# Optimization experiments

Hardware: AMD Instinct MI355X
Metric: run time of the kernel (lower is better)

## Reference

```python
import jax, jax.numpy as jnp
import numpy as np

N_NODES = 100000
N_EDGES = 1600000
D_FEAT = 48


def setup_inputs() -> dict:
    key = jax.random.key(0)
    k1, k2, k3, k4 = jax.random.split(key, 4)
    rows = jax.random.randint(k1, (N_EDGES,), 0, N_NODES, dtype=jnp.int32)
    cols = jax.random.randint(k2, (N_EDGES,), 0, N_NODES, dtype=jnp.int32)
    # normalized adjacency values (positive, like D^-1/2 A D^-1/2 entries)
    vals = jax.random.uniform(k3, (N_EDGES,), dtype=jnp.float32)
    embeds = jax.random.normal(k4, (N_NODES, D_FEAT), dtype=jnp.float32)
    return {"rows": rows, "cols": cols, "vals": vals, "embeds": embeds}


def reference(rows, cols, vals, embeds):
    # torch.spmm(adj, embeds) with adj in COO form:
    # out[i] = sum_{e : rows[e]==i} vals[e] * embeds[cols[e]]
    msgs = vals[:, None] * embeds[cols]          # [E, D] gather + scale
    out = jax.ops.segment_sum(msgs, rows, num_segments=embeds.shape[0])  # [N, D]
    return out
```

## Files before the change

### kernel.cpp

```cpp
#include <hip/hip_runtime.h>


#define N_NODES 100000
#define D_FEAT 48
#define DQ (D_FEAT / 4)
#define DQ4 (D_FEAT / 8)

#define BUCKET_BITS 7
#define BUCKET_NODES 128
#define N_BUCKETS ((N_NODES + BUCKET_NODES - 1) / BUCKET_NODES)
#define CAPB 2432

#define CHUNK 8192
#define P1_THREADS 1024
#define VPT (CHUNK / P1_THREADS / 4)

#define P2_THREADS 768
#define EPT2 ((CAPB + P2_THREADS - 1) / P2_THREADS)
#define NG6 (P2_THREADS / 6)

#define OVF_CAP 4096
#define EBF_UINT2 (N_NODES * DQ)

typedef float  fl32x4 __attribute__((ext_vector_type(4)));
typedef unsigned long long u64;

__device__ __forceinline__ unsigned short f2bf(float f) {
    unsigned u = __float_as_uint(f);
    return (unsigned short)((u + 0x7FFFu + ((u >> 16) & 1u)) >> 16);
}

__device__ __forceinline__ float4 bf2f4(uint2 h) {
    float4 m;
    m.x = __uint_as_float((h.x & 0xFFFFu) << 16);
    m.y = __uint_as_float(h.x & 0xFFFF0000u);
    m.z = __uint_as_float((h.y & 0xFFFFu) << 16);
    m.w = __uint_as_float(h.y & 0xFFFF0000u);
    return m;
}

__global__ __launch_bounds__(P1_THREADS) void partition_kernel(
        const int* __restrict__ rows, const int* __restrict__ cols,
        const float* __restrict__ vals, int* __restrict__ gcur,
        uint2* __restrict__ tmp, uint4* __restrict__ ovf, int* __restrict__ novf,
        const float* __restrict__ embeds, uint2* __restrict__ ebf,
        int n_edges) {
    __shared__ int counts[N_BUCKETS];
    __shared__ int starts[N_BUCKETS];
    __shared__ int cursor[N_BUCKETS];
    __shared__ int adj[N_BUCKETS];
    __shared__ int wtot[16];
    __shared__ unsigned lkey[CHUNK];
    __shared__ unsigned lval[CHUNK];
    __shared__ int      ldst[CHUNK];

    int t = threadIdx.x;
    int lane = t & 63;
    int wid = t >> 6;
    int base = blockIdx.x * CHUNK;
    int n = min(CHUNK, n_edges - base);
    int n4 = n >> 2;

    for (int i = t; i < N_BUCKETS; i += P1_THREADS) counts[i] = 0;
    __syncthreads();

    int      b[VPT * 4];
    unsigned key[VPT * 4];
    float    v[VPT * 4];
    const int4*   rows4 = reinterpret_cast<const int4*>(rows + base);
    const int4*   cols4 = reinterpret_cast<const int4*>(cols + base);
    const float4* vals4 = reinterpret_cast<const float4*>(vals + base);
#pragma unroll
    for (int k = 0; k < VPT; ++k) {
        int idx4 = k * P1_THREADS + t;
        bool ok = idx4 < n4;
        int4   r4 = ok ? rows4[idx4] : make_int4(0, 0, 0, 0);
        int4   c4 = ok ? cols4[idx4] : make_int4(0, 0, 0, 0);
        float4 v4 = ok ? vals4[idx4] : make_float4(0.f, 0.f, 0.f, 0.f);
        int rr[4] = {r4.x, r4.y, r4.z, r4.w};
        int cc[4] = {c4.x, c4.y, c4.z, c4.w};
        float vv[4] = {v4.x, v4.y, v4.z, v4.w};
#pragma unroll
        for (int j = 0; j < 4; ++j) {
            int i = k * 4 + j;
            b[i] = -1;
            if (ok) {
                b[i] = rr[j] >> BUCKET_BITS;
                key[i] = ((unsigned)(rr[j] & (BUCKET_NODES - 1)) << 17) | (unsigned)cc[j];
                v[i] = vv[j];
                atomicAdd(&counts[b[i]], 1);
            }
        }
    }

    if (ebf) {
        const float4* e4 = reinterpret_cast<const float4*>(embeds);
        int stride = gridDim.x * P1_THREADS;
        for (int i = blockIdx.x * P1_THREADS + t; i < EBF_UINT2; i += stride) {
            float4 f = e4[i];
            uint2 p;
            p.x = (unsigned)f2bf(f.x) | ((unsigned)f2bf(f.y) << 16);
            p.y = (unsigned)f2bf(f.z) | ((unsigned)f2bf(f.w) << 16);
            ebf[i] = p;
        }
    }
    __syncthreads();

    int cnt_t = (t < N_BUCKETS) ? counts[t] : 0;
    int x = cnt_t;
#pragma unroll
    for (int d = 1; d < 64; d <<= 1) {
        int y = __shfl_up(x, d, 64);
        if (lane >= d) x += y;
    }
    if (lane == 63) wtot[wid] = x;
    __syncthreads();
    if (t < 64) {
        int w = (t < 16) ? wtot[t] : 0;
        int xs = w;
#pragma unroll
        for (int d = 1; d < 16; d <<= 1) {
            int y = __shfl_up(xs, d, 64);
            if (lane >= d) xs += y;
        }
        if (t < 16) wtot[t] = xs - w;
    }
    __syncthreads();
    if (t < N_BUCKETS) {
        int excl = x - cnt_t + wtot[wid];
        starts[t] = excl;
        cursor[t] = excl;
        int gp = (cnt_t > 0) ? atomicAdd(&gcur[t], cnt_t) : 0;
        adj[t] = t * CAPB + gp - excl;
    }
    __syncthreads();

#pragma unroll
    for (int i = 0; i < VPT * 4; ++i) {
        if (b[i] >= 0) {
            int p = atomicAdd(&cursor[b[i]], 1);
            int dest = adj[b[i]] + p;
            if (dest < (b[i] + 1) * CAPB) {
                lkey[p] = key[i];
                lval[p] = __float_as_uint(v[i]);
                ldst[p] = dest;
            } else {
                ldst[p] = -1;
                int o = atomicAdd(novf, 1);
                if (o < OVF_CAP) {
                    unsigned rl = key[i] >> 17;
                    ovf[o] = make_uint4((unsigned)b[i] * BUCKET_NODES + rl,
                                        key[i] & 0x1FFFFu, __float_as_uint(v[i]), 0u);
                }
            }
        }
    }
    __syncthreads();

    u64* tmp8 = reinterpret_cast<u64*>(tmp);
    for (int i = t; i < n; i += P1_THREADS) {
        int d = ldst[i];
        if (d >= 0)
            tmp8[d] = (u64)lkey[i] | ((u64)lval[i] << 32);
    }
}

#define ACCUM_OVF_TAIL(GATHER_EXPR)                                             \
    {                                                                           \
        int nov = min(*novf, OVF_CAP);                                          \
        if (nov > 0) {                                                          \
            __syncthreads();                                                    \
            int lo = bkt * BUCKET_NODES, hi = lo + BUCKET_NODES;                \
            for (int i = t; i < nov; i += P2_THREADS) {                         \
                uint4 en = ovf[i];                                              \
                int node = (int)en.x;                                           \
                if (node >= lo && node < hi && node < N_NODES) {                \
                    unsigned c = en.y;                                          \
                    float v = __uint_as_float(en.z);                            \
                    for (int qq = 0; qq < DQ; ++qq) {                           \
                        float4 m = GATHER_EXPR;                                 \
                        float* dst = out + (size_t)node * D_FEAT + qq * 4;      \
                        atomicAdd(dst + 0, v * m.x);                            \
                        atomicAdd(dst + 1, v * m.y);                            \
                        atomicAdd(dst + 2, v * m.z);                            \
                        atomicAdd(dst + 3, v * m.w);                            \
                    }                                                           \
                }                                                               \
            }                                                                   \
        }                                                                       \
    }

__global__ __launch_bounds__(P2_THREADS) void accum_bf16_kernel(
        const int* __restrict__ gcur, const uint2* __restrict__ tmp,
        const uint2* __restrict__ ebf, float* __restrict__ out,
        const int* __restrict__ novf, const uint4* __restrict__ ovf) {
    __shared__ uint2 sorted[CAPB];
    __shared__ int cnt[BUCKET_NODES];
    __shared__ int cur[BUCKET_NODES];
    __shared__ int roff[BUCKET_NODES + 1];
    __shared__ int ws2[2];

    int t = threadIdx.x;
    int lane = t & 63;
    int bkt = blockIdx.x;
    const uint2* bucket = tmp + (size_t)bkt * CAPB;
    int cntE = min(gcur[bkt], CAPB);

    if (t < BUCKET_NODES) cnt[t] = 0;
    __syncthreads();

    unsigned kcol[EPT2]; unsigned vbits[EPT2]; int erl[EPT2];
#pragma unroll
    for (int j = 0; j < EPT2; ++j) {
        int idx = t + j * P2_THREADS;
        erl[j] = -1;
        if (idx < cntE) {
            u64 pk8 = __builtin_nontemporal_load(
                reinterpret_cast<const u64*>(bucket) + idx);
            unsigned kx = (unsigned)pk8;
            erl[j] = (int)(kx >> 17);
            kcol[j] = kx & 0x1FFFFu;
            vbits[j] = (unsigned)(pk8 >> 32);
            atomicAdd(&cnt[erl[j]], 1);
        }
    }
    __syncthreads();

    int x = 0;
    if (t < BUCKET_NODES) {
        x = cnt[t];
#pragma unroll
        for (int d = 1; d < 64; d <<= 1) {
            int y = __shfl_up(x, d, 64);
            if (lane >= d) x += y;
        }
        if (lane == 63) ws2[t >> 6] = x;
    }
    __syncthreads();
    if (t == 0) { int a = ws2[0]; ws2[0] = 0; ws2[1] = a; }
    __syncthreads();
    if (t < BUCKET_NODES) {
        int incl = x + ws2[t >> 6];
        int st = incl - cnt[t];
        roff[t] = st; cur[t] = st;
    }
    if (t == 0) roff[BUCKET_NODES] = cntE;
    __syncthreads();

#pragma unroll
    for (int j = 0; j < EPT2; ++j) {
        if (erl[j] >= 0) {
            int pos = atomicAdd(&cur[erl[j]], 1);
            sorted[pos] = make_uint2(kcol[j], vbits[j]);
        }
    }
    __syncthreads();

    int g = t / 6, q = t - g * 6;
    {
        const uint4* ebq = reinterpret_cast<const uint4*>(ebf) + q;
        int rl = g;
        int e = roff[rl], e1 = roff[rl + 1];
        float4 aA = make_float4(0.f, 0.f, 0.f, 0.f);
        float4 aB = make_float4(0.f, 0.f, 0.f, 0.f);
        for (; e + 3 < e1; e += 4) {
            uint2 p0 = sorted[e],     p1 = sorted[e + 1];
            uint2 p2 = sorted[e + 2], p3 = sorted[e + 3];
            uint4 h0 = ebq[p0.x * DQ4];
            uint4 h1 = ebq[p1.x * DQ4];
            uint4 h2 = ebq[p2.x * DQ4];
            uint4 h3 = ebq[p3.x * DQ4];
            float v0 = __uint_as_float(p0.y), v1 = __uint_as_float(p1.y);
            float v2 = __uint_as_float(p2.y), v3 = __uint_as_float(p3.y);
            float4 mA0 = bf2f4(make_uint2(h0.x, h0.y)), mB0 = bf2f4(make_uint2(h0.z, h0.w));
            float4 mA1 = bf2f4(make_uint2(h1.x, h1.y)), mB1 = bf2f4(make_uint2(h1.z, h1.w));
            float4 mA2 = bf2f4(make_uint2(h2.x, h2.y)), mB2 = bf2f4(make_uint2(h2.z, h2.w));
            float4 mA3 = bf2f4(make_uint2(h3.x, h3.y)), mB3 = bf2f4(make_uint2(h3.z, h3.w));
            aA.x += v0 * mA0.x; aA.y += v0 * mA0.y; aA.z += v0 * mA0.z; aA.w += v0 * mA0.w;
            aB.x += v0 * mB0.x; aB.y += v0 * mB0.y; aB.z += v0 * mB0.z; aB.w += v0 * mB0.w;
            aA.x += v1 * mA1.x; aA.y += v1 * mA1.y; aA.z += v1 * mA1.z; aA.w += v1 * mA1.w;
            aB.x += v1 * mB1.x; aB.y += v1 * mB1.y; aB.z += v1 * mB1.z; aB.w += v1 * mB1.w;
            aA.x += v2 * mA2.x; aA.y += v2 * mA2.y; aA.z += v2 * mA2.z; aA.w += v2 * mA2.w;
            aB.x += v2 * mB2.x; aB.y += v2 * mB2.y; aB.z += v2 * mB2.z; aB.w += v2 * mB2.w;
            aA.x += v3 * mA3.x; aA.y += v3 * mA3.y; aA.z += v3 * mA3.z; aA.w += v3 * mA3.w;
            aB.x += v3 * mB3.x; aB.y += v3 * mB3.y; aB.z += v3 * mB3.z; aB.w += v3 * mB3.w;
        }
        for (; e < e1; ++e) {
            uint2 p0 = sorted[e];
            uint4 h0 = ebq[p0.x * DQ4];
            float v0 = __uint_as_float(p0.y);
            float4 mA0 = bf2f4(make_uint2(h0.x, h0.y)), mB0 = bf2f4(make_uint2(h0.z, h0.w));
            aA.x += v0 * mA0.x; aA.y += v0 * mA0.y; aA.z += v0 * mA0.z; aA.w += v0 * mA0.w;
            aB.x += v0 * mB0.x; aB.y += v0 * mB0.y; aB.z += v0 * mB0.z; aB.w += v0 * mB0.w;
        }
        int node = bkt * BUCKET_NODES + rl;
        if (node < N_NODES) {
            float* dst = out + (size_t)node * D_FEAT + q * 8;
            fl32x4 A = {aA.x, aA.y, aA.z, aA.w};
            fl32x4 B = {aB.x, aB.y, aB.z, aB.w};
            __builtin_nontemporal_store(A, reinterpret_cast<fl32x4*>(dst));
            __builtin_nontemporal_store(B, reinterpret_cast<fl32x4*>(dst + 4));
        }
    }
    ACCUM_OVF_TAIL(bf2f4(ebf[c * DQ + qq]))
}

__global__ __launch_bounds__(P2_THREADS) void accum_f32_kernel(
        const int* __restrict__ gcur, const uint2* __restrict__ tmp,
        const float* __restrict__ embeds, float* __restrict__ out,
        const int* __restrict__ novf, const uint4* __restrict__ ovf) {
    __shared__ uint2 sorted[CAPB];
    __shared__ int cnt[BUCKET_NODES];
    __shared__ int cur[BUCKET_NODES];
    __shared__ int roff[BUCKET_NODES + 1];
    __shared__ int ws2[2];
    int t = threadIdx.x;
    int lane = t & 63;
    int bkt = blockIdx.x;
    const uint2* bucket = tmp + (size_t)bkt * CAPB;
    int cntE = min(gcur[bkt], CAPB);
    if (t < BUCKET_NODES) cnt[t] = 0;
    __syncthreads();
    unsigned kcol[EPT2]; unsigned vbits[EPT2]; int erl[EPT2];
#pragma unroll
    for (int j = 0; j < EPT2; ++j) {
        int idx = t + j * P2_THREADS;
        erl[j] = -1;
        if (idx < cntE) {
            uint2 pk = bucket[idx];
            erl[j] = (int)(pk.x >> 17);
            kcol[j] = pk.x & 0x1FFFFu;
            vbits[j] = pk.y;
            atomicAdd(&cnt[erl[j]], 1);
        }
    }
    __syncthreads();
    int x = 0;
    if (t < BUCKET_NODES) {
        x = cnt[t];
#pragma unroll
        for (int d = 1; d < 64; d <<= 1) {
            int y = __shfl_up(x, d, 64);
            if (lane >= d) x += y;
        }
        if (lane == 63) ws2[t >> 6] = x;
    }
    __syncthreads();
    if (t == 0) { int a = ws2[0]; ws2[0] = 0; ws2[1] = a; }
    __syncthreads();
    if (t < BUCKET_NODES) {
        int incl = x + ws2[t >> 6];
        int st = incl - cnt[t];
        roff[t] = st; cur[t] = st;
    }
    if (t == 0) roff[BUCKET_NODES] = cntE;
    __syncthreads();
#pragma unroll
    for (int j = 0; j < EPT2; ++j) {
        if (erl[j] >= 0) {
            int p = atomicAdd(&cur[erl[j]], 1);
            sorted[p] = make_uint2(kcol[j], vbits[j]);
        }
    }
    __syncthreads();
    int g = t / 12;
    int q = t - g * 12;
    if (g < P2_THREADS / 12) {
        for (int rl = g; rl < BUCKET_NODES; rl += P2_THREADS / 12) {
            int s = roff[rl], epos = roff[rl + 1];
            float4 a0 = make_float4(0.f, 0.f, 0.f, 0.f);
            int e = s;
            for (; e < epos; ++e) {
                uint2 p0 = sorted[e];
                float4 m0 = *(reinterpret_cast<const float4*>(embeds + p0.x * D_FEAT) + q);
                float v0 = __uint_as_float(p0.y);
                a0.x += v0 * m0.x; a0.y += v0 * m0.y; a0.z += v0 * m0.z; a0.w += v0 * m0.w;
            }
            int node = bkt * BUCKET_NODES + rl;
            if (node < N_NODES)
                *(reinterpret_cast<float4*>(out + (size_t)node * D_FEAT) + q) = a0;
        }
    }
    ACCUM_OVF_TAIL((*(reinterpret_cast<const float4*>(embeds + (size_t)c * D_FEAT) + qq)))
}

extern "C" void kernel_launch(void* const* d_in, const int* in_sizes, int n_in,
                              void* d_out, int out_size, void* d_ws, size_t ws_size,
                              hipStream_t stream) {
    const int*   rows   = (const int*)d_in[0];
    const int*   cols   = (const int*)d_in[1];
    const float* vals   = (const float*)d_in[2];
    const float* embeds = (const float*)d_in[3];
    float*       out    = (float*)d_out;
    int n_edges = in_sizes[0];

    const size_t TMP_OFF = 4096 + 65536;
    const size_t TMP_SZ  = (size_t)N_BUCKETS * CAPB * sizeof(uint2);
    const size_t EBF_OFF = TMP_OFF + TMP_SZ;
    const size_t EBF_SZ  = (size_t)EBF_UINT2 * sizeof(uint2);
    char* ws = (char*)d_ws;
    int*   gcur = (int*)(ws);
    int*   novf = (int*)(ws + 3200);
    uint4* ovf  = (uint4*)(ws + 4096);
    uint2* tmp  = (uint2*)(ws + TMP_OFF);
    uint2* ebf  = (uint2*)(ws + EBF_OFF);

    bool use_bf16 = ws_size >= EBF_OFF + EBF_SZ;

    hipMemsetAsync(ws, 0, 3264, stream);

    int p1_blocks = (n_edges + CHUNK - 1) / CHUNK;
    partition_kernel<<<p1_blocks, P1_THREADS, 0, stream>>>(
        rows, cols, vals, gcur, tmp, ovf, novf,
        embeds, use_bf16 ? ebf : (uint2*)nullptr, n_edges);

    if (use_bf16)
        accum_bf16_kernel<<<N_BUCKETS, P2_THREADS, 0, stream>>>(gcur, tmp, ebf, out, novf, ovf);
    else
        accum_f32_kernel<<<N_BUCKETS, P2_THREADS, 0, stream>>>(gcur, tmp, embeds, out, novf, ovf);
}
```

Measured before the change: 132.2 us.

## Replace global atomic bucket cursors with fixed per-block slots and byte counts

The partition kernel no longer reserves bucket space through global atomicAdd on a shared cursor. Each chunk block instead writes into a fixed SLOTS-sized region per bucket and records its per-bucket count as a byte. The accumulate kernel reads those counts and scans the padded slot layout, skipping empty slots. This removes the global atomics and the larger memset, at the cost of a sparser tmp layout (nblk*SLOTS entries per bucket), more overflow-path traffic whenever a block's bucket count exceeds SLOTS, and per-edge slot checks in phase two.

```diff
diff --git a/kernel.cpp b/kernel.cpp
--- a/kernel.cpp
+++ b/kernel.cpp
@@ -10,14 +10,15 @@
 #define BUCKET_NODES 128
 #define N_BUCKETS ((N_NODES + BUCKET_NODES - 1) / BUCKET_NODES)
 #define CAPB 2432
+#define SLOTS 20
 
 #define CHUNK 8192
 #define P1_THREADS 1024
 #define VPT (CHUNK / P1_THREADS / 4)
 
 #define P2_THREADS 768
-#define EPT2 ((CAPB + P2_THREADS - 1) / P2_THREADS)
-#define NG6 (P2_THREADS / 6)
+#define EPT3 6
+#define NBLK_MAX 256
 
 #define OVF_CAP 4096
 #define EBF_UINT2 (N_NODES * DQ)
@@ -41,14 +42,13 @@
 
 __global__ __launch_bounds__(P1_THREADS) void partition_kernel(
         const int* __restrict__ rows, const int* __restrict__ cols,
-        const float* __restrict__ vals, int* __restrict__ gcur,
+        const float* __restrict__ vals, unsigned char* __restrict__ cnts,
         uint2* __restrict__ tmp, uint4* __restrict__ ovf, int* __restrict__ novf,
         const float* __restrict__ embeds, uint2* __restrict__ ebf,
-        int n_edges) {
+        int n_edges, int nblk) {
     __shared__ int counts[N_BUCKETS];
-    __shared__ int starts[N_BUCKETS];
     __shared__ int cursor[N_BUCKETS];
-    __shared__ int adj[N_BUCKETS];
+    __shared__ int2 adjlim[N_BUCKETS];
     __shared__ int wtot[16];
     __shared__ unsigned lkey[CHUNK];
     __shared__ unsigned lval[CHUNK];
@@ -57,7 +57,8 @@
     int t = threadIdx.x;
     int lane = t & 63;
     int wid = t >> 6;
-    int base = blockIdx.x * CHUNK;
+    int blk = blockIdx.x;
+    int base = blk * CHUNK;
     int n = min(CHUNK, n_edges - base);
     int n4 = n >> 2;
 
@@ -96,7 +97,7 @@
     if (ebf) {
         const float4* e4 = reinterpret_cast<const float4*>(embeds);
         int stride = gridDim.x * P1_THREADS;
-        for (int i = blockIdx.x * P1_THREADS + t; i < EBF_UINT2; i += stride) {
+        for (int i = blk * P1_THREADS + t; i < EBF_UINT2; i += stride) {
             float4 f = e4[i];
             uint2 p;
             p.x = (unsigned)f2bf(f.x) | ((unsigned)f2bf(f.y) << 16);
@@ -128,10 +129,10 @@
     __syncthreads();
     if (t < N_BUCKETS) {
         int excl = x - cnt_t + wtot[wid];
-        starts[t] = excl;
         cursor[t] = excl;
-        int gp = (cnt_t > 0) ? atomicAdd(&gcur[t], cnt_t) : 0;
-        adj[t] = t * CAPB + gp - excl;
+        int rbase = t * (nblk * SLOTS) + blk * SLOTS;
+        adjlim[t] = make_int2(rbase - excl, rbase + SLOTS);
+        counts[t] = min(cnt_t, SLOTS);
     }
     __syncthreads();
 
@@ -139,8 +140,9 @@
     for (int i = 0; i < VPT * 4; ++i) {
         if (b[i] >= 0) {
             int p = atomicAdd(&cursor[b[i]], 1);
-            int dest = adj[b[i]] + p;
-            if (dest < (b[i] + 1) * CAPB) {
+            int2 al = adjlim[b[i]];
+            int dest = al.x + p;
+            if (dest < al.y) {
                 lkey[p] = key[i];
                 lval[p] = __float_as_uint(v[i]);
                 ldst[p] = dest;
@@ -163,6 +165,9 @@
         if (d >= 0)
             tmp8[d] = (u64)lkey[i] | ((u64)lval[i] << 32);
     }
+
+    for (int i = t; i < N_BUCKETS; i += P1_THREADS)
+        cnts[blk * N_BUCKETS + i] = (unsigned char)counts[i];
 }
 
 #define ACCUM_OVF_TAIL(GATHER_EXPR)                                             \
@@ -191,37 +196,42 @@
     }
 
 __global__ __launch_bounds__(P2_THREADS) void accum_bf16_kernel(
-        const int* __restrict__ gcur, const uint2* __restrict__ tmp,
+        const unsigned char* __restrict__ cnts, const uint2* __restrict__ tmp,
         const uint2* __restrict__ ebf, float* __restrict__ out,
-        const int* __restrict__ novf, const uint4* __restrict__ ovf) {
+        const int* __restrict__ novf, const uint4* __restrict__ ovf, int nblk) {
     __shared__ uint2 sorted[CAPB];
     __shared__ int cnt[BUCKET_NODES];
     __shared__ int cur[BUCKET_NODES];
     __shared__ int roff[BUCKET_NODES + 1];
     __shared__ int ws2[2];
+    __shared__ int scnt[NBLK_MAX];
 
     int t = threadIdx.x;
     int lane = t & 63;
     int bkt = blockIdx.x;
-    const uint2* bucket = tmp + (size_t)bkt * CAPB;
-    int cntE = min(gcur[bkt], CAPB);
+    int S = nblk * SLOTS;
+    const u64* bbase = reinterpret_cast<const u64*>(tmp) + (size_t)bkt * S;
 
     if (t < BUCKET_NODES) cnt[t] = 0;
-    __syncthreads();
-
-    unsigned kcol[EPT2]; unsigned vbits[EPT2]; int erl[EPT2];
-#pragma unroll
-    for (int j = 0; j < EPT2; ++j) {
+    for (int i = t; i < nblk; i += P2_THREADS) scnt[i] = cnts[i * N_BUCKETS + bkt];
+    __syncthreads();
+
+    unsigned kcol[EPT3]; unsigned vbits[EPT3]; int erl[EPT3];
+#pragma unroll
+    for (int j = 0; j < EPT3; ++j) {
         int idx = t + j * P2_THREADS;
         erl[j] = -1;
-        if (idx < cntE) {
-            u64 pk8 = __builtin_nontemporal_load(
-                reinterpret_cast<const u64*>(bucket) + idx);
-            unsigned kx = (unsigned)pk8;
-            erl[j] = (int)(kx >> 17);
-            kcol[j] = kx & 0x1FFFFu;
-            vbits[j] = (unsigned)(pk8 >> 32);
-            atomicAdd(&cnt[erl[j]], 1);
+        if (idx < S) {
+            int bb = idx / SLOTS;
+            int slot = idx - bb * SLOTS;
+            if (slot < scnt[bb]) {
+                u64 pk8 = __builtin_nontemporal_load(bbase + idx);
+                unsigned kx = (unsigned)pk8;
+                erl[j] = (int)(kx >> 17);
+                kcol[j] = kx & 0x1FFFFu;
+                vbits[j] = (unsigned)(pk8 >> 32);
+                atomicAdd(&cnt[erl[j]], 1);
+            }
         }
     }
     __syncthreads();
@@ -244,14 +254,20 @@
         int st = incl - cnt[t];
         roff[t] = st; cur[t] = st;
     }
-    if (t == 0) roff[BUCKET_NODES] = cntE;
-    __syncthreads();
-
-#pragma unroll
-    for (int j = 0; j < EPT2; ++j) {
+    if (t == 0) roff[BUCKET_NODES] = 0;
+    __syncthreads();
+    if (t == 0) roff[BUCKET_NODES] = ws2[1] + ((BUCKET_NODES > 64) ? 0 : 0);
+    if (t == 0) {
+        roff[BUCKET_NODES] = roff[BUCKET_NODES - 1] + cnt[BUCKET_NODES - 1];
+    }
+    __syncthreads();
+
+#pragma unroll
+    for (int j = 0; j < EPT3; ++j) {
         if (erl[j] >= 0) {
             int pos = atomicAdd(&cur[erl[j]], 1);
-            sorted[pos] = make_uint2(kcol[j], vbits[j]);
+            if (pos < CAPB)
+                sorted[pos] = make_uint2(kcol[j], vbits[j]);
         }
     }
     __syncthreads();
@@ -260,7 +276,8 @@
     {
         const uint4* ebq = reinterpret_cast<const uint4*>(ebf) + q;
         int rl = g;
-        int e = roff[rl], e1 = roff[rl + 1];
+        int e1 = min(roff[rl + 1], CAPB);
+        int e = min(roff[rl], e1);
         float4 aA = make_float4(0.f, 0.f, 0.f, 0.f);
         float4 aB = make_float4(0.f, 0.f, 0.f, 0.f);
         for (; e + 3 < e1; e += 4) {
@@ -306,32 +323,39 @@
 }
 
 __global__ __launch_bounds__(P2_THREADS) void accum_f32_kernel(
-        const int* __restrict__ gcur, const uint2* __restrict__ tmp,
+        const unsigned char* __restrict__ cnts, const uint2* __restrict__ tmp,
         const float* __restrict__ embeds, float* __restrict__ out,
-        const int* __restrict__ novf, const uint4* __restrict__ ovf) {
+        const int* __restrict__ novf, const uint4* __restrict__ ovf, int nblk) {
     __shared__ uint2 sorted[CAPB];
     __shared__ int cnt[BUCKET_NODES];
     __shared__ int cur[BUCKET_NODES];
     __shared__ int roff[BUCKET_NODES + 1];
     __shared__ int ws2[2];
+    __shared__ int scnt[NBLK_MAX];
     int t = threadIdx.x;
     int lane = t & 63;
     int bkt = blockIdx.x;
-    const uint2* bucket = tmp + (size_t)bkt * CAPB;
-    int cntE = min(gcur[bkt], CAPB);
+    int S = nblk * SLOTS;
+    const u64* bbase = reinterpret_cast<const u64*>(tmp) + (size_t)bkt * S;
     if (t < BUCKET_NODES) cnt[t] = 0;
-    __syncthreads();
-    unsigned kcol[EPT2]; unsigned vbits[EPT2]; int erl[EPT2];
-#pragma unroll
-    for (int j = 0; j < EPT2; ++j) {
+    for (int i = t; i < nblk; i += P2_THREADS) scnt[i] = cnts[i * N_BUCKETS + bkt];
+    __syncthreads();
+    unsigned kcol[EPT3]; unsigned vbits[EPT3]; int erl[EPT3];
+#pragma unroll
+    for (int j = 0; j < EPT3; ++j) {
         int idx = t + j * P2_THREADS;
         erl[j] = -1;
-        if (idx < cntE) {
-            uint2 pk = bucket[idx];
-            erl[j] = (int)(pk.x >> 17);
-            kcol[j] = pk.x & 0x1FFFFu;
-            vbits[j] = pk.y;
-            atomicAdd(&cnt[erl[j]], 1);
+        if (idx < S) {
+            int bb = idx / SLOTS;
+            int slot = idx - bb * SLOTS;
+            if (slot < scnt[bb]) {
+                u64 pk8 = bbase[idx];
+                unsigned kx = (unsigned)pk8;
+                erl[j] = (int)(kx >> 17);
+                kcol[j] = kx & 0x1FFFFu;
+                vbits[j] = (unsigned)(pk8 >> 32);
+                atomicAdd(&cnt[erl[j]], 1);
+            }
         }
     }
     __syncthreads();
@@ -353,13 +377,15 @@
         int st = incl - cnt[t];
         roff[t] = st; cur[t] = st;
     }
-    if (t == 0) roff[BUCKET_NODES] = cntE;
-    __syncthreads();
-#pragma unroll
-    for (int j = 0; j < EPT2; ++j) {
+    __syncthreads();
+    if (t == 0) roff[BUCKET_NODES] = roff[BUCKET_NODES - 1] + cnt[BUCKET_NODES - 1];
+    __syncthreads();
+#pragma unroll
+    for (int j = 0; j < EPT3; ++j) {
         if (erl[j] >= 0) {
             int p = atomicAdd(&cur[erl[j]], 1);
-            sorted[p] = make_uint2(kcol[j], vbits[j]);
+            if (p < CAPB)
+                sorted[p] = make_uint2(kcol[j], vbits[j]);
         }
     }
     __syncthreads();
@@ -367,9 +393,9 @@
     int q = t - g * 12;
     if (g < P2_THREADS / 12) {
         for (int rl = g; rl < BUCKET_NODES; rl += P2_THREADS / 12) {
-            int s = roff[rl], epos = roff[rl + 1];
+            int epos = min(roff[rl + 1], CAPB);
+            int e = min(roff[rl], epos);
             float4 a0 = make_float4(0.f, 0.f, 0.f, 0.f);
-            int e = s;
             for (; e < epos; ++e) {
                 uint2 p0 = sorted[e];
                 float4 m0 = *(reinterpret_cast<const float4*>(embeds + p0.x * D_FEAT) + q);
@@ -394,28 +420,34 @@
     float*       out    = (float*)d_out;
     int n_edges = in_sizes[0];
 
-    const size_t TMP_OFF = 4096 + 65536;
-    const size_t TMP_SZ  = (size_t)N_BUCKETS * CAPB * sizeof(uint2);
-    const size_t EBF_OFF = TMP_OFF + TMP_SZ;
-    const size_t EBF_SZ  = (size_t)EBF_UINT2 * sizeof(uint2);
+    int nblk = (n_edges + CHUNK - 1) / CHUNK;
+    if (nblk > NBLK_MAX) nblk = NBLK_MAX;
+
+    const size_t OVF_OFF  = 4096;
+    const size_t CNTS_OFF = OVF_OFF + (size_t)OVF_CAP * 16;
+    const size_t TMP_OFF  = 270336;
+    const size_t TMP_SZ   = (size_t)N_BUCKETS * nblk * SLOTS * 8;
+    const size_t EBF_OFF  = TMP_OFF + TMP_SZ;
+    const size_t EBF_SZ   = (size_t)EBF_UINT2 * sizeof(uint2);
     char* ws = (char*)d_ws;
-    int*   gcur = (int*)(ws);
-    int*   novf = (int*)(ws + 3200);
-    uint4* ovf  = (uint4*)(ws + 4096);
-    uint2* tmp  = (uint2*)(ws + TMP_OFF);
-    uint2* ebf  = (uint2*)(ws + EBF_OFF);
+    int*           novf = (int*)(ws);
+    uint4*         ovf  = (uint4*)(ws + OVF_OFF);
+    unsigned char* cnts = (unsigned char*)(ws + CNTS_OFF);
+    uint2*         tmp  = (uint2*)(ws + TMP_OFF);
+    uint2*         ebf  = (uint2*)(ws + EBF_OFF);
 
     bool use_bf16 = ws_size >= EBF_OFF + EBF_SZ;
 
-    hipMemsetAsync(ws, 0, 3264, stream);
-
-    int p1_blocks = (n_edges + CHUNK - 1) / CHUNK;
-    partition_kernel<<<p1_blocks, P1_THREADS, 0, stream>>>(
-        rows, cols, vals, gcur, tmp, ovf, novf,
-        embeds, use_bf16 ? ebf : (uint2*)nullptr, n_edges);
+    hipMemsetAsync(ws, 0, 256, stream);
+
+    partition_kernel<<<nblk, P1_THREADS, 0, stream>>>(
+        rows, cols, vals, cnts, tmp, ovf, novf,
+        embeds, use_bf16 ? ebf : (uint2*)nullptr, n_edges, nblk);
 
     if (use_bf16)
-        accum_bf16_kernel<<<N_BUCKETS, P2_THREADS, 0, stream>>>(gcur, tmp, ebf, out, novf, ovf);
+        accum_bf16_kernel<<<N_BUCKETS, P2_THREADS, 0, stream>>>(
+            cnts, tmp, ebf, out, novf, ovf, nblk);
     else
-        accum_f32_kernel<<<N_BUCKETS, P2_THREADS, 0, stream>>>(gcur, tmp, embeds, out, novf, ovf);
-}
+        accum_f32_kernel<<<N_BUCKETS, P2_THREADS, 0, stream>>>(
+            cnts, tmp, embeds, out, novf, ovf, nblk);
+}
```

Measured after the change: 146.5 us. +10.8%, slower.
